# Kernel optimization log

Hardware: AMD Instinct MI355X
Metric: run time of the kernel (lower is better)

The kernel has to match this reference:

```python
import jax, jax.numpy as jnp
import numpy as np

EMBED_DIM = 768
NUM_HEADS = 12
HEAD_DIM = EMBED_DIM // NUM_HEADS
B, S = 2, 2048


def setup_inputs() -> dict:
    key = jax.random.key(0)
    k1, k2, k3, k4, k5 = jax.random.split(key, 5)
    scale = 1.0 / np.sqrt(EMBED_DIM)
    return {
        "x": jax.random.normal(k1, (B, S, EMBED_DIM), dtype=jnp.float32),
        "w_qkv": jax.random.normal(k2, (EMBED_DIM, 3 * EMBED_DIM), dtype=jnp.float32) * scale,
        "b_qkv": jax.random.normal(k3, (3 * EMBED_DIM,), dtype=jnp.float32) * 0.01,
        "w_proj": jax.random.normal(k4, (EMBED_DIM, EMBED_DIM), dtype=jnp.float32) * scale,
        "b_proj": jax.random.normal(k5, (EMBED_DIM,), dtype=jnp.float32) * 0.01,
    }


def reference(x, w_qkv, b_qkv, w_proj, b_proj):
    b, s, e = x.shape
    h, d = NUM_HEADS, HEAD_DIM
    # fused QKV projection: [b, s, 3, h, d]
    qkv = (x @ w_qkv + b_qkv).reshape(b, s, 3, h, d)
    q = qkv[:, :, 0].transpose(0, 2, 1, 3)  # [b, h, s, d]
    k = qkv[:, :, 1].transpose(0, 2, 1, 3)
    v = qkv[:, :, 2].transpose(0, 2, 1, 3)
    scores = jnp.einsum("bhqd,bhkd->bhqk", q, k) * (d ** -0.5)
    attn = jax.nn.softmax(scores, axis=-1)  # dropout is identity in eval mode
    out = jnp.einsum("bhqk,bhkd->bhqd", attn, v)
    out = out.transpose(0, 2, 1, 3).reshape(b, s, e)
    return out @ w_proj + b_proj
```

## Files before the change

### kernel.cpp

```cpp
#include <hip/hip_runtime.h>
#include <hip/hip_bf16.h>


typedef __bf16 bf16x8 __attribute__((ext_vector_type(8)));
typedef float f32x4 __attribute__((ext_vector_type(4)));
typedef unsigned short ushortx8 __attribute__((ext_vector_type(8)));
typedef unsigned short ushortx4 __attribute__((ext_vector_type(4)));

#define EMB 768
#define SEQ 2048
#define NHEAD 12
#define HDIM 64
#define MROWS 4096
#define NQKV 2304
#define QSCALE 0.18033688011112042f

static __device__ __forceinline__ unsigned short b16(float f) {
  __hip_bfloat16 h = __float2bfloat16(f);
  return __builtin_bit_cast(unsigned short, h);
}

static __device__ __forceinline__ void gld16(const void* g, void* l) {
  __builtin_amdgcn_global_load_lds((const __attribute__((address_space(1))) void*)g,
                                   (__attribute__((address_space(3))) void*)l, 16, 0, 0);
}

__global__ __launch_bounds__(256) void k_prep(
    const float* __restrict__ x, const float* __restrict__ wqkv, const float* __restrict__ wproj,
    unsigned short* __restrict__ xb, unsigned short* __restrict__ wqkvT,
    unsigned short* __restrict__ wprojT) {
  __shared__ float t[64][65];
  const int bid = blockIdx.x;
  const int tid = threadIdx.x;
  if (bid < 1536) {
    int i = (bid * 256 + tid) * 8;
    f32x4 v0 = *(const f32x4*)(x + i);
    f32x4 v1 = *(const f32x4*)(x + i + 4);
    ushortx8 o;
    o[0] = b16(v0[0]); o[1] = b16(v0[1]); o[2] = b16(v0[2]); o[3] = b16(v0[3]);
    o[4] = b16(v1[0]); o[5] = b16(v1[1]); o[6] = b16(v1[2]); o[7] = b16(v1[3]);
    *(ushortx8*)(xb + i) = o;
    return;
  }
  const float* in; unsigned short* out; int N, bx, by;
  if (bid < 1536 + 432) { in = wqkv;  out = wqkvT;  N = NQKV; int r = bid - 1536; bx = r % 36; by = r / 36; }
  else                  { in = wproj; out = wprojT; N = EMB;  int r = bid - 1968; bx = r % 12; by = r / 12; }
  const int n0 = bx * 64, k0 = by * 64;
  const int xx = tid & 63, y0 = tid >> 6;
  #pragma unroll
  for (int i = 0; i < 16; ++i) { int r = y0 * 16 + i; t[r][xx] = in[(size_t)(k0 + r) * N + n0 + xx]; }
  __syncthreads();
  const int ks = tid & 7;
  const int nr0 = tid >> 3;
  #pragma unroll
  for (int i = 0; i < 2; ++i) {
    int nr = nr0 + i * 32;
    ushortx8 o;
    #pragma unroll
    for (int j = 0; j < 8; ++j) o[j] = b16(t[ks * 8 + j][nr]);
    *(ushortx8*)(out + (size_t)(n0 + nr) * EMB + k0 + ks * 8) = o;
  }
}

static __device__ __forceinline__ void gemm_tile_128(
    const unsigned short* __restrict__ A, const unsigned short* __restrict__ B,
    int K, int bm, int bn, char* lA, char* lB, f32x4 acc[4][4]) {
  const int tid = threadIdx.x, lane = tid & 63, w = tid >> 6;
  const int l15 = lane & 15, lg = lane >> 4;
  const int wm = w >> 1, wn = w & 1;
  #pragma unroll
  for (int m = 0; m < 4; ++m)
    #pragma unroll
    for (int n = 0; n < 4; ++n)
      acc[m][n] = (f32x4){0.f, 0.f, 0.f, 0.f};

  const int srow = w * 32 + (lane >> 3);
  const int glog = (lane & 7) ^ (lane >> 3);
  const size_t abase = (size_t)(bm * 128 + srow) * K + glog * 8;
  const size_t bbase = (size_t)(bn * 128 + srow) * K + glog * 8;
  const char* aB = lA + (wm * 64 + l15) * 128;
  const char* bB = lB + (wn * 64 + l15) * 128;
  const int rsw = (l15 & 7) << 4;

  const int T = K >> 6;
  {
    char* ad = lA + w * 4096; char* bd = lB + w * 4096;
    #pragma unroll
    for (int j = 0; j < 4; ++j) {
      gld16(A + abase + (size_t)j * 8 * K, ad + j * 1024);
      gld16(B + bbase + (size_t)j * 8 * K, bd + j * 1024);
    }
  }
  for (int t = 0; t < T; ++t) {
    const int cur = t & 1;
    if (t + 1 < T) {
      const int k1 = (t + 1) << 6;
      char* ad = lA + (cur ^ 1) * 16384 + w * 4096;
      char* bd = lB + (cur ^ 1) * 16384 + w * 4096;
      #pragma unroll
      for (int j = 0; j < 4; ++j) {
        gld16(A + abase + (size_t)j * 8 * K + k1, ad + j * 1024);
        gld16(B + bbase + (size_t)j * 8 * K + k1, bd + j * 1024);
      }
      asm volatile("s_waitcnt vmcnt(8)" ::: "memory");
    } else {
      asm volatile("s_waitcnt vmcnt(0)" ::: "memory");
    }
    __builtin_amdgcn_s_barrier();
    const char* ab = aB + cur * 16384;
    const char* bb = bB + cur * 16384;
    bf16x8 af[2][4], bfr[2][4];
    #pragma unroll
    for (int kk = 0; kk < 2; ++kk) {
      #pragma unroll
      for (int m = 0; m < 4; ++m)
        af[kk][m] = *(const bf16x8*)(ab + m * 2048 + (((kk * 4 + lg) * 16) ^ rsw));
      #pragma unroll
      for (int n = 0; n < 4; ++n)
        bfr[kk][n] = *(const bf16x8*)(bb + n * 2048 + (((kk * 4 + lg) * 16) ^ rsw));
    }
    #pragma unroll
    for (int kk = 0; kk < 2; ++kk)
      #pragma unroll
      for (int m = 0; m < 4; ++m)
        #pragma unroll
        for (int n = 0; n < 4; ++n)
          acc[m][n] = __builtin_amdgcn_mfma_f32_16x16x32_bf16(af[kk][m], bfr[kk][n], acc[m][n], 0, 0, 0);
    if (t + 1 < T) __builtin_amdgcn_s_barrier();
  }
}

static __device__ __forceinline__ int kvperm(int s) {
  return (s & ~0x1C) | ((s & 0x0C) << 1) | ((s & 0x10) >> 2);
}

__global__ __launch_bounds__(256) void k_gemm_qkv(
    const unsigned short* __restrict__ Xb, const unsigned short* __restrict__ Wt,
    const float* __restrict__ bias,
    unsigned short* __restrict__ Qb, unsigned short* __restrict__ Kb,
    unsigned short* __restrict__ VTb) {
  __shared__ __align__(16) char Alds[2 * 16384];
  __shared__ __align__(16) char Blds[2 * 16384];
  f32x4 acc[4][4];
  const int bm = blockIdx.x, bn = blockIdx.y;
  gemm_tile_128(Xb, Wt, EMB, bm, bn, Alds, Blds, acc);
  const int tid = threadIdx.x, lane = tid & 63, w = tid >> 6;
  const int l15 = lane & 15, lg = lane >> 4, wm = w >> 1, wn = w & 1;
  const int treg = bn / 6;
  if (treg < 2) {
    #pragma unroll
    for (int m = 0; m < 4; ++m)
      #pragma unroll
      for (int n = 0; n < 4; ++n)
        #pragma unroll
        for (int r = 0; r < 4; ++r) {
          int gr = bm * 128 + wm * 64 + m * 16 + lg * 4 + r;
          int gc = bn * 128 + wn * 64 + n * 16 + l15;
          float v = acc[m][n][r] + bias[gc];
          int rem = gc - treg * 768;
          int h = rem >> 6, d = rem & 63;
          int b = gr >> 11, s = gr & 2047;
          size_t off = ((size_t)(b * 12 + h) * 2048 + s) * 64 + d;
          if (treg == 0) Qb[off] = b16(v * QSCALE);
          else           Kb[off] = b16(v);
        }
  } else {
    #pragma unroll
    for (int m = 0; m < 4; ++m)
      #pragma unroll
      for (int n = 0; n < 4; ++n) {
        int gr0 = bm * 128 + wm * 64 + m * 16 + lg * 4;
        int gc = bn * 128 + wn * 64 + n * 16 + l15;
        int rem = gc - 1536;
        int h = rem >> 6, d = rem & 63;
        int b = gr0 >> 11, s0 = gr0 & 2047;
        int sp0 = kvperm(s0);
        ushortx4 o;
        #pragma unroll
        for (int r = 0; r < 4; ++r) o[r] = b16(acc[m][n][r] + bias[gc]);
        *(ushortx4*)(VTb + ((size_t)(b * 12 + h) * 64 + d) * 2048 + sp0) = o;
      }
  }
}

__global__ __launch_bounds__(256) void k_gemm_proj(
    const unsigned short* __restrict__ Ab, const unsigned short* __restrict__ Wt,
    const float* __restrict__ bias, float* __restrict__ out) {
  __shared__ __align__(16) char Alds[2 * 16384];
  __shared__ __align__(16) char Blds[2 * 16384];
  f32x4 acc[4][4];
  const int bm = blockIdx.x, bn = blockIdx.y;
  gemm_tile_128(Ab, Wt, EMB, bm, bn, Alds, Blds, acc);
  const int tid = threadIdx.x, lane = tid & 63, w = tid >> 6;
  const int l15 = lane & 15, lg = lane >> 4, wm = w >> 1, wn = w & 1;
  #pragma unroll
  for (int m = 0; m < 4; ++m)
    #pragma unroll
    for (int n = 0; n < 4; ++n)
      #pragma unroll
      for (int r = 0; r < 4; ++r) {
        int gr = bm * 128 + wm * 64 + m * 16 + lg * 4 + r;
        int gc = bn * 128 + wn * 64 + n * 16 + l15;
        out[(size_t)gr * EMB + gc] = acc[m][n][r] + bias[gc];
      }
}

__global__ __launch_bounds__(256) void k_attn(
    const unsigned short* __restrict__ Qg, const unsigned short* __restrict__ Kg,
    const unsigned short* __restrict__ VTg, unsigned short* __restrict__ AO) {
  __shared__ __align__(16) char KL[3 * 8192];
  __shared__ __align__(16) char VTL[3 * 8192];
  const int bid = blockIdx.x;
  const int slot = bid >> 3;
  const int bh = (bid & 7) * 3 + slot / 32;
  const int qt = slot & 31;
  const int b = bh / 12, h = bh % 12;
  const size_t base = (size_t)bh * (SEQ * HDIM);
  const int tid = threadIdx.x, lane = tid & 63, w = tid >> 6;
  const int l15 = lane & 15, lg = lane >> 4;
  const int swz = (l15 & 7) << 4;

  bf16x8 qf[2];
  {
    const size_t qoff = base + (size_t)(qt * 64 + w * 16 + l15) * 64 + lg * 8;
    qf[0] = *(const bf16x8*)(Qg + qoff);
    qf[1] = *(const bf16x8*)(Qg + qoff + 32);
  }

  const int srow0 = tid >> 3;
  const int scg0 = (tid & 7) ^ (srow0 & 7);
  const int scg1 = (tid & 7) ^ ((srow0 + 32) & 7);

  #define ASTAGE(tt, buf) do {                                                         \
    const int kv_ = (tt) * 64;                                                         \
    char* kd_ = KL + (buf) * 8192 + w * 1024;                                          \
    char* vd_ = VTL + (buf) * 8192 + w * 1024;                                         \
    gld16(Kg + base + (size_t)(kv_ + srow0) * 64 + scg0 * 8,           kd_);           \
    gld16(Kg + base + (size_t)(kv_ + srow0 + 32) * 64 + scg1 * 8,      kd_ + 4096);    \
    gld16(VTg + base + (size_t)srow0 * 2048 + kv_ + scg0 * 8,          vd_);           \
    gld16(VTg + base + (size_t)(srow0 + 32) * 2048 + kv_ + scg1 * 8,   vd_ + 4096);    \
  } while (0)

  f32x4 Oacc[4];
  #pragma unroll
  for (int nd = 0; nd < 4; ++nd) Oacc[nd] = (f32x4){0.f, 0.f, 0.f, 0.f};
  float l_ = 0.f;

  ASTAGE(0, 0);
  ASTAGE(1, 1);
  asm volatile("s_waitcnt vmcnt(4)" ::: "memory");
  __builtin_amdgcn_s_barrier();

  int cur = 0, pre = 2;
  for (int t = 0; t < 32; ++t) {
    if (t + 2 < 32) ASTAGE(t + 2, pre);
    const char* kb = KL + cur * 8192;
    const char* vb = VTL + cur * 8192;

    f32x4 sv[4];
    __builtin_amdgcn_s_setprio(1);
    #pragma unroll
    for (int n = 0; n < 4; ++n) {
      const char* rb = kb + (n * 16 + l15) * 128;
      bf16x8 kf0 = *(const bf16x8*)(rb + ((lg * 16) ^ swz));
      bf16x8 kf1 = *(const bf16x8*)(rb + ((64 + lg * 16) ^ swz));
      f32x4 z = (f32x4){0.f, 0.f, 0.f, 0.f};
      z = __builtin_amdgcn_mfma_f32_16x16x32_bf16(kf0, qf[0], z, 0, 0, 0);
      sv[n] = __builtin_amdgcn_mfma_f32_16x16x32_bf16(kf1, qf[1], z, 0, 0, 0);
    }

    #pragma unroll
    for (int c = 0; c < 2; ++c) {
      ushortx8 up;
      #pragma unroll
      for (int j = 0; j < 4; ++j) {
        float pa = __builtin_amdgcn_exp2f(sv[2 * c][j]);
        float pb = __builtin_amdgcn_exp2f(sv[2 * c + 1][j]);
        l_ += pa + pb;
        up[j] = b16(pa);
        up[4 + j] = b16(pb);
      }
      bf16x8 pfB = __builtin_bit_cast(bf16x8, up);
      #pragma unroll
      for (int nd = 0; nd < 4; ++nd) {
        const char* vr = vb + (nd * 16 + l15) * 128;
        bf16x8 vf = *(const bf16x8*)(vr + ((c * 64 + lg * 16) ^ swz));
        Oacc[nd] = __builtin_amdgcn_mfma_f32_16x16x32_bf16(vf, pfB, Oacc[nd], 0, 0, 0);
      }
    }
    __builtin_amdgcn_s_setprio(0);

    if (t < 31) {
      if (t < 30) asm volatile("s_waitcnt vmcnt(4)" ::: "memory");
      else        asm volatile("s_waitcnt vmcnt(0)" ::: "memory");
      __builtin_amdgcn_s_barrier();
    }
    cur = (cur == 2) ? 0 : cur + 1;
    pre = (pre == 2) ? 0 : pre + 1;
  }
  #undef ASTAGE

  l_ += __shfl_xor(l_, 16);
  l_ += __shfl_xor(l_, 32);
  const float rl = 1.0f / l_;
  const int q = qt * 64 + w * 16 + l15;
  #pragma unroll
  for (int nd = 0; nd < 4; ++nd) {
    ushortx4 o;
    #pragma unroll
    for (int r = 0; r < 4; ++r) o[r] = b16(Oacc[nd][r] * rl);
    *(ushortx4*)(AO + ((size_t)(b * 2048 + q)) * EMB + h * 64 + nd * 16 + lg * 4) = o;
  }
}

extern "C" void kernel_launch(void* const* d_in, const int* in_sizes, int n_in,
                              void* d_out, int out_size, void* d_ws, size_t ws_size,
                              hipStream_t stream) {
  const float* x     = (const float*)d_in[0];
  const float* wqkv  = (const float*)d_in[1];
  const float* bqkv  = (const float*)d_in[2];
  const float* wproj = (const float*)d_in[3];
  const float* bproj = (const float*)d_in[4];
  float* out = (float*)d_out;
  char* ws = (char*)d_ws;

  unsigned short* xb     = (unsigned short*)(ws + 0);
  unsigned short* wqkvT  = (unsigned short*)(ws + 6291456);
  unsigned short* wprojT = (unsigned short*)(ws + 9830400);
  unsigned short* Qb     = (unsigned short*)(ws + 11010048);
  unsigned short* Kb     = (unsigned short*)(ws + 17301504);
  unsigned short* VTb    = (unsigned short*)(ws + 23592960);
  unsigned short* AOb    = (unsigned short*)(ws + 29884416);

  k_prep<<<2112, 256, 0, stream>>>(x, wqkv, wproj, xb, wqkvT, wprojT);
  k_gemm_qkv<<<dim3(MROWS / 128, NQKV / 128), 256, 0, stream>>>(xb, wqkvT, bqkv, Qb, Kb, VTb);
  k_attn<<<24 * (SEQ / 64), 256, 0, stream>>>(Qb, Kb, VTb, AOb);
  k_gemm_proj<<<dim3(MROWS / 128, EMB / 128), 256, 0, stream>>>(AOb, wprojT, bproj, out);
}
```

Before: 89.21 us.

## Compute softmax row sums via MFMA with ones and remap GEMM block order per XCD

The attention kernel no longer sums the exponentiated scores with scalar adds and cross-lane shuffles. Instead it issues one extra MFMA per chunk that multiplies a bf16 ones vector by the P fragment, so the row sums land in an accumulator. This moves VALU adds off the exp path at the cost of MFMA work and summing bf16-rounded probabilities. Both GEMM kernels also switch to a 1D grid with a swizzled block-to-tile mapping, so that blocks placed on the same XCD share row tiles and reuse L2.

```diff
diff --git a/kernel.cpp b/kernel.cpp
--- a/kernel.cpp
+++ b/kernel.cpp
@@ -142,7 +142,10 @@
   __shared__ __align__(16) char Alds[2 * 16384];
   __shared__ __align__(16) char Blds[2 * 16384];
   f32x4 acc[4][4];
-  const int bm = blockIdx.x, bn = blockIdx.y;
+  const int id = blockIdx.x;
+  const int kq = id >> 3;
+  const int bn = kq % 18;
+  const int bm = (id & 7) * 4 + kq / 18;
   gemm_tile_128(Xb, Wt, EMB, bm, bn, Alds, Blds, acc);
   const int tid = threadIdx.x, lane = tid & 63, w = tid >> 6;
   const int l15 = lane & 15, lg = lane >> 4, wm = w >> 1, wn = w & 1;
@@ -189,7 +192,10 @@
   __shared__ __align__(16) char Alds[2 * 16384];
   __shared__ __align__(16) char Blds[2 * 16384];
   f32x4 acc[4][4];
-  const int bm = blockIdx.x, bn = blockIdx.y;
+  const int id = blockIdx.x;
+  const int kq = id >> 3;
+  const int bn = kq % 6;
+  const int bm = (id & 7) * 4 + kq / 6;
   gemm_tile_128(Ab, Wt, EMB, bm, bn, Alds, Blds, acc);
   const int tid = threadIdx.x, lane = tid & 63, w = tid >> 6;
   const int l15 = lane & 15, lg = lane >> 4, wm = w >> 1, wn = w & 1;
@@ -241,10 +247,15 @@
     gld16(VTg + base + (size_t)(srow0 + 32) * 2048 + kv_ + scg1 * 8,   vd_ + 4096);    \
   } while (0)
 
+  ushortx8 os;
+  #pragma unroll
+  for (int j = 0; j < 8; ++j) os[j] = 0x3F80;
+  const bf16x8 onesf = __builtin_bit_cast(bf16x8, os);
+
   f32x4 Oacc[4];
   #pragma unroll
   for (int nd = 0; nd < 4; ++nd) Oacc[nd] = (f32x4){0.f, 0.f, 0.f, 0.f};
-  float l_ = 0.f;
+  f32x4 Lacc = (f32x4){0.f, 0.f, 0.f, 0.f};
 
   ASTAGE(0, 0);
   ASTAGE(1, 1);
@@ -274,13 +285,11 @@
       ushortx8 up;
       #pragma unroll
       for (int j = 0; j < 4; ++j) {
-        float pa = __builtin_amdgcn_exp2f(sv[2 * c][j]);
-        float pb = __builtin_amdgcn_exp2f(sv[2 * c + 1][j]);
-        l_ += pa + pb;
-        up[j] = b16(pa);
-        up[4 + j] = b16(pb);
+        up[j]     = b16(__builtin_amdgcn_exp2f(sv[2 * c][j]));
+        up[4 + j] = b16(__builtin_amdgcn_exp2f(sv[2 * c + 1][j]));
       }
       bf16x8 pfB = __builtin_bit_cast(bf16x8, up);
+      Lacc = __builtin_amdgcn_mfma_f32_16x16x32_bf16(onesf, pfB, Lacc, 0, 0, 0);
       #pragma unroll
       for (int nd = 0; nd < 4; ++nd) {
         const char* vr = vb + (nd * 16 + l15) * 128;
@@ -300,9 +309,7 @@
   }
   #undef ASTAGE
 
-  l_ += __shfl_xor(l_, 16);
-  l_ += __shfl_xor(l_, 32);
-  const float rl = 1.0f / l_;
+  const float rl = 1.0f / Lacc[0];
   const int q = qt * 64 + w * 16 + l15;
   #pragma unroll
   for (int nd = 0; nd < 4; ++nd) {
@@ -333,7 +340,7 @@
   unsigned short* AOb    = (unsigned short*)(ws + 29884416);
 
   k_prep<<<2112, 256, 0, stream>>>(x, wqkv, wproj, xb, wqkvT, wprojT);
-  k_gemm_qkv<<<dim3(MROWS / 128, NQKV / 128), 256, 0, stream>>>(xb, wqkvT, bqkv, Qb, Kb, VTb);
+  k_gemm_qkv<<<576, 256, 0, stream>>>(xb, wqkvT, bqkv, Qb, Kb, VTb);
   k_attn<<<24 * (SEQ / 64), 256, 0, stream>>>(Qb, Kb, VTb, AOb);
-  k_gemm_proj<<<dim3(MROWS / 128, EMB / 128), 256, 0, stream>>>(AOb, wprojT, bproj, out);
-}
+  k_gemm_proj<<<192, 256, 0, stream>>>(AOb, wprojT, bproj, out);
+}
```

Result: no change. 90.98 us (+2.0%).

## Split attention waves over query and key halves to reuse K/V fragments

Applied to the files above, without the earlier changes.

Each wave of the attention kernel now covers 32 query rows and half of each 64-key tile instead of 16 query rows and the full tile. Every K and V fragment read from LDS therefore feeds two query blocks, which halves the LDS read traffic per MFMA. The partial outputs and row sums from the two key halves are combined through LDS in an epilogue, which adds a reduction step and extra accumulator registers. The probabilities are also packed to bf16 with a v_cvt_pk_bf16_f32 instruction that converts two floats at once, in place of separate per-element conversions.

```diff
diff --git a/kernel.cpp b/kernel.cpp
--- a/kernel.cpp
+++ b/kernel.cpp
@@ -6,6 +6,7 @@
 typedef float f32x4 __attribute__((ext_vector_type(4)));
 typedef unsigned short ushortx8 __attribute__((ext_vector_type(8)));
 typedef unsigned short ushortx4 __attribute__((ext_vector_type(4)));
+typedef unsigned int uintx4 __attribute__((ext_vector_type(4)));
 
 #define EMB 768
 #define SEQ 2048
@@ -18,6 +19,12 @@
 static __device__ __forceinline__ unsigned short b16(float f) {
   __hip_bfloat16 h = __float2bfloat16(f);
   return __builtin_bit_cast(unsigned short, h);
+}
+
+static __device__ __forceinline__ unsigned int cvtpk(float lo, float hi) {
+  unsigned int r;
+  asm("v_cvt_pk_bf16_f32 %0, %1, %2" : "=v"(r) : "v"(lo), "v"(hi));
+  return r;
 }
 
 static __device__ __forceinline__ void gld16(const void* g, void* l) {
@@ -208,8 +215,9 @@
 __global__ __launch_bounds__(256) void k_attn(
     const unsigned short* __restrict__ Qg, const unsigned short* __restrict__ Kg,
     const unsigned short* __restrict__ VTg, unsigned short* __restrict__ AO) {
-  __shared__ __align__(16) char KL[3 * 8192];
-  __shared__ __align__(16) char VTL[3 * 8192];
+  __shared__ __align__(16) char LDSbuf[49152];
+  char* KL  = LDSbuf;
+  char* VTL = LDSbuf + 24576;
   const int bid = blockIdx.x;
   const int slot = bid >> 3;
   const int bh = (bid & 7) * 3 + slot / 32;
@@ -218,13 +226,16 @@
   const size_t base = (size_t)bh * (SEQ * HDIM);
   const int tid = threadIdx.x, lane = tid & 63, w = tid >> 6;
   const int l15 = lane & 15, lg = lane >> 4;
+  const int qh = w >> 1, kh = w & 1;
   const int swz = (l15 & 7) << 4;
 
-  bf16x8 qf[2];
+  bf16x8 qf[2][2];
   {
-    const size_t qoff = base + (size_t)(qt * 64 + w * 16 + l15) * 64 + lg * 8;
-    qf[0] = *(const bf16x8*)(Qg + qoff);
-    qf[1] = *(const bf16x8*)(Qg + qoff + 32);
+    const size_t qoff = base + (size_t)(qt * 64 + qh * 32 + l15) * 64 + lg * 8;
+    qf[0][0] = *(const bf16x8*)(Qg + qoff);
+    qf[0][1] = *(const bf16x8*)(Qg + qoff + 32);
+    qf[1][0] = *(const bf16x8*)(Qg + qoff + 1024);
+    qf[1][1] = *(const bf16x8*)(Qg + qoff + 1024 + 32);
   }
 
   const int srow0 = tid >> 3;
@@ -241,10 +252,12 @@
     gld16(VTg + base + (size_t)(srow0 + 32) * 2048 + kv_ + scg1 * 8,   vd_ + 4096);    \
   } while (0)
 
-  f32x4 Oacc[4];
-  #pragma unroll
-  for (int nd = 0; nd < 4; ++nd) Oacc[nd] = (f32x4){0.f, 0.f, 0.f, 0.f};
-  float l_ = 0.f;
+  f32x4 acc[2][4];
+  #pragma unroll
+  for (int n = 0; n < 2; ++n)
+    #pragma unroll
+    for (int nd = 0; nd < 4; ++nd) acc[n][nd] = (f32x4){0.f, 0.f, 0.f, 0.f};
+  float lsum[2] = {0.f, 0.f};
 
   ASTAGE(0, 0);
   ASTAGE(1, 1);
@@ -257,36 +270,48 @@
     const char* kb = KL + cur * 8192;
     const char* vb = VTL + cur * 8192;
 
-    f32x4 sv[4];
     __builtin_amdgcn_s_setprio(1);
-    #pragma unroll
-    for (int n = 0; n < 4; ++n) {
-      const char* rb = kb + (n * 16 + l15) * 128;
-      bf16x8 kf0 = *(const bf16x8*)(rb + ((lg * 16) ^ swz));
-      bf16x8 kf1 = *(const bf16x8*)(rb + ((64 + lg * 16) ^ swz));
-      f32x4 z = (f32x4){0.f, 0.f, 0.f, 0.f};
-      z = __builtin_amdgcn_mfma_f32_16x16x32_bf16(kf0, qf[0], z, 0, 0, 0);
-      sv[n] = __builtin_amdgcn_mfma_f32_16x16x32_bf16(kf1, qf[1], z, 0, 0, 0);
-    }
-
-    #pragma unroll
-    for (int c = 0; c < 2; ++c) {
-      ushortx8 up;
-      #pragma unroll
-      for (int j = 0; j < 4; ++j) {
-        float pa = __builtin_amdgcn_exp2f(sv[2 * c][j]);
-        float pb = __builtin_amdgcn_exp2f(sv[2 * c + 1][j]);
-        l_ += pa + pb;
-        up[j] = b16(pa);
-        up[4 + j] = b16(pb);
+    bf16x8 kf[2][2], vf[4];
+    #pragma unroll
+    for (int n2 = 0; n2 < 2; ++n2) {
+      const char* rb = kb + (kh * 32 + n2 * 16 + l15) * 128;
+      kf[n2][0] = *(const bf16x8*)(rb + ((lg * 16) ^ swz));
+      kf[n2][1] = *(const bf16x8*)(rb + ((64 + lg * 16) ^ swz));
+    }
+    #pragma unroll
+    for (int nd = 0; nd < 4; ++nd)
+      vf[nd] = *(const bf16x8*)(vb + (nd * 16 + l15) * 128 + ((kh * 64 + lg * 16) ^ swz));
+
+    f32x4 sv[2][2];
+    #pragma unroll
+    for (int n = 0; n < 2; ++n)
+      #pragma unroll
+      for (int n2 = 0; n2 < 2; ++n2) {
+        f32x4 z = (f32x4){0.f, 0.f, 0.f, 0.f};
+        z = __builtin_amdgcn_mfma_f32_16x16x32_bf16(kf[n2][0], qf[n][0], z, 0, 0, 0);
+        sv[n][n2] = __builtin_amdgcn_mfma_f32_16x16x32_bf16(kf[n2][1], qf[n][1], z, 0, 0, 0);
       }
-      bf16x8 pfB = __builtin_bit_cast(bf16x8, up);
-      #pragma unroll
-      for (int nd = 0; nd < 4; ++nd) {
-        const char* vr = vb + (nd * 16 + l15) * 128;
-        bf16x8 vf = *(const bf16x8*)(vr + ((c * 64 + lg * 16) ^ swz));
-        Oacc[nd] = __builtin_amdgcn_mfma_f32_16x16x32_bf16(vf, pfB, Oacc[nd], 0, 0, 0);
-      }
+
+    #pragma unroll
+    for (int n = 0; n < 2; ++n) {
+      float p0 = __builtin_amdgcn_exp2f(sv[n][0][0]);
+      float p1 = __builtin_amdgcn_exp2f(sv[n][0][1]);
+      float p2 = __builtin_amdgcn_exp2f(sv[n][0][2]);
+      float p3 = __builtin_amdgcn_exp2f(sv[n][0][3]);
+      float p4 = __builtin_amdgcn_exp2f(sv[n][1][0]);
+      float p5 = __builtin_amdgcn_exp2f(sv[n][1][1]);
+      float p6 = __builtin_amdgcn_exp2f(sv[n][1][2]);
+      float p7 = __builtin_amdgcn_exp2f(sv[n][1][3]);
+      lsum[n] += ((p0 + p1) + (p2 + p3)) + ((p4 + p5) + (p6 + p7));
+      uintx4 uw;
+      uw[0] = cvtpk(p0, p1);
+      uw[1] = cvtpk(p2, p3);
+      uw[2] = cvtpk(p4, p5);
+      uw[3] = cvtpk(p6, p7);
+      bf16x8 pf = __builtin_bit_cast(bf16x8, uw);
+      #pragma unroll
+      for (int nd = 0; nd < 4; ++nd)
+        acc[n][nd] = __builtin_amdgcn_mfma_f32_16x16x32_bf16(vf[nd], pf, acc[n][nd], 0, 0, 0);
     }
     __builtin_amdgcn_s_setprio(0);
 
@@ -300,16 +325,39 @@
   }
   #undef ASTAGE
 
-  l_ += __shfl_xor(l_, 16);
-  l_ += __shfl_xor(l_, 32);
-  const float rl = 1.0f / l_;
-  const int q = qt * 64 + w * 16 + l15;
-  #pragma unroll
-  for (int nd = 0; nd < 4; ++nd) {
-    ushortx4 o;
-    #pragma unroll
-    for (int r = 0; r < 4; ++r) o[r] = b16(Oacc[nd][r] * rl);
-    *(ushortx4*)(AO + ((size_t)(b * 2048 + q)) * EMB + h * 64 + nd * 16 + lg * 4) = o;
+  #pragma unroll
+  for (int n = 0; n < 2; ++n) {
+    lsum[n] += __shfl_xor(lsum[n], 16);
+    lsum[n] += __shfl_xor(lsum[n], 32);
+  }
+  __syncthreads();
+  float* scr = (float*)LDSbuf;
+  float* lscr = scr + 8192;
+  #pragma unroll
+  for (int n = 0; n < 2; ++n)
+    #pragma unroll
+    for (int nd = 0; nd < 4; ++nd)
+      *(f32x4*)(scr + ((w * 2 + n) * 4 + nd) * 256 + lane * 4) = acc[n][nd];
+  if (lane < 16) {
+    lscr[w * 32 + l15] = lsum[0];
+    lscr[w * 32 + 16 + l15] = lsum[1];
+  }
+  __syncthreads();
+  {
+    const int pw = w ^ 1;
+    const int n = kh;
+    const float lp = lscr[pw * 32 + n * 16 + l15];
+    const float rl = 1.0f / (lsum[n] + lp);
+    const int q = qt * 64 + qh * 32 + n * 16 + l15;
+    unsigned short* aor = AO + ((size_t)(b * 2048 + q)) * EMB + h * 64;
+    #pragma unroll
+    for (int nd = 0; nd < 4; ++nd) {
+      f32x4 part = *(const f32x4*)(scr + ((pw * 2 + n) * 4 + nd) * 256 + lane * 4);
+      ushortx4 o;
+      #pragma unroll
+      for (int r = 0; r < 4; ++r) o[r] = b16((acc[n][nd][r] + part[r]) * rl);
+      *(ushortx4*)(aor + nd * 16 + lg * 4) = o;
+    }
   }
 }
 
```

After: 92.30 us. 3.5% more time.

## Use 64x64 tiles with XCD-aware block mapping in output projection GEMM

Applied to the files above, without the earlier changes.

Replaces the 128x128-tile projection GEMM (192 blocks) with a dedicated 64x64-tile kernel launched as 768 blocks, so more of the GPU's compute units get work. Block ids are remapped so that consecutive ids spread across the 8 XCDs while each XCD handles a contiguous range of rows, which should improve L2 reuse. The kernel keeps double-buffered direct-to-LDS loads with a swizzle. The cost is more redundant A/B loads per output element and a smaller MFMA count per barrier.

```diff
diff --git a/kernel.cpp b/kernel.cpp
--- a/kernel.cpp
+++ b/kernel.cpp
@@ -186,21 +186,83 @@
 __global__ __launch_bounds__(256) void k_gemm_proj(
     const unsigned short* __restrict__ Ab, const unsigned short* __restrict__ Wt,
     const float* __restrict__ bias, float* __restrict__ out) {
-  __shared__ __align__(16) char Alds[2 * 16384];
-  __shared__ __align__(16) char Blds[2 * 16384];
-  f32x4 acc[4][4];
-  const int bm = blockIdx.x, bn = blockIdx.y;
-  gemm_tile_128(Ab, Wt, EMB, bm, bn, Alds, Blds, acc);
+  __shared__ __align__(16) char Alds[2 * 8192];
+  __shared__ __align__(16) char Blds[2 * 8192];
+  const int id = blockIdx.x;
+  const int k = id >> 3;
+  const int bn = k % 12;
+  const int bm = (id & 7) * 8 + k / 12;
   const int tid = threadIdx.x, lane = tid & 63, w = tid >> 6;
-  const int l15 = lane & 15, lg = lane >> 4, wm = w >> 1, wn = w & 1;
-  #pragma unroll
-  for (int m = 0; m < 4; ++m)
-    #pragma unroll
-    for (int n = 0; n < 4; ++n)
+  const int l15 = lane & 15, lg = lane >> 4;
+  const int wm = w >> 1, wn = w & 1;
+  f32x4 acc[2][2];
+  #pragma unroll
+  for (int m = 0; m < 2; ++m)
+    #pragma unroll
+    for (int n = 0; n < 2; ++n)
+      acc[m][n] = (f32x4){0.f, 0.f, 0.f, 0.f};
+
+  const int srow = w * 8 + (lane >> 3);
+  const int glog = (lane & 7) ^ (lane >> 3);
+  const size_t abase  = (size_t)(bm * 64 + srow) * EMB + glog * 8;
+  const size_t abase2 = abase + (size_t)32 * EMB;
+  const size_t bbase  = (size_t)(bn * 64 + srow) * EMB + glog * 8;
+  const size_t bbase2 = bbase + (size_t)32 * EMB;
+  const char* aB = (char*)Alds + (wm * 32 + l15) * 128;
+  const char* bB = (char*)Blds + (wn * 32 + l15) * 128;
+  const int rsw = (l15 & 7) << 4;
+
+  #define G2STAGE(k1, buf) do {                                          \
+    char* ad_ = (char*)Alds + (buf) * 8192 + w * 1024;                   \
+    char* bd_ = (char*)Blds + (buf) * 8192 + w * 1024;                   \
+    gld16(Ab + abase + (k1), ad_);                                       \
+    gld16(Ab + abase2 + (k1), ad_ + 4096);                               \
+    gld16(Wt + bbase + (k1), bd_);                                       \
+    gld16(Wt + bbase2 + (k1), bd_ + 4096);                               \
+  } while (0)
+
+  G2STAGE(0, 0);
+  const int T = EMB >> 6;
+  for (int t = 0; t < T; ++t) {
+    const int cur = t & 1;
+    if (t + 1 < T) {
+      G2STAGE((t + 1) << 6, cur ^ 1);
+      asm volatile("s_waitcnt vmcnt(4)" ::: "memory");
+    } else {
+      asm volatile("s_waitcnt vmcnt(0)" ::: "memory");
+    }
+    __builtin_amdgcn_s_barrier();
+    const char* ab = aB + cur * 8192;
+    const char* bb = bB + cur * 8192;
+    bf16x8 af[2][2], bfr[2][2];
+    #pragma unroll
+    for (int kk = 0; kk < 2; ++kk) {
+      #pragma unroll
+      for (int m = 0; m < 2; ++m)
+        af[kk][m] = *(const bf16x8*)(ab + m * 2048 + (((kk * 4 + lg) * 16) ^ rsw));
+      #pragma unroll
+      for (int n = 0; n < 2; ++n)
+        bfr[kk][n] = *(const bf16x8*)(bb + n * 2048 + (((kk * 4 + lg) * 16) ^ rsw));
+    }
+    #pragma unroll
+    for (int kk = 0; kk < 2; ++kk)
+      #pragma unroll
+      for (int m = 0; m < 2; ++m)
+        #pragma unroll
+        for (int n = 0; n < 2; ++n)
+          acc[m][n] = __builtin_amdgcn_mfma_f32_16x16x32_bf16(af[kk][m], bfr[kk][n], acc[m][n], 0, 0, 0);
+    if (t + 1 < T) __builtin_amdgcn_s_barrier();
+  }
+  #undef G2STAGE
+
+  #pragma unroll
+  for (int m = 0; m < 2; ++m)
+    #pragma unroll
+    for (int n = 0; n < 2; ++n)
       #pragma unroll
       for (int r = 0; r < 4; ++r) {
-        int gr = bm * 128 + wm * 64 + m * 16 + lg * 4 + r;
-        int gc = bn * 128 + wn * 64 + n * 16 + l15;
+        int gr = bm * 64 + wm * 32 + m * 16 + lg * 4 + r;
+        int gc = bn * 64 + wn * 32 + n * 16 + l15;
         out[(size_t)gr * EMB + gc] = acc[m][n][r] + bias[gc];
       }
 }
@@ -335,5 +397,5 @@
   k_prep<<<2112, 256, 0, stream>>>(x, wqkv, wproj, xb, wqkvT, wprojT);
   k_gemm_qkv<<<dim3(MROWS / 128, NQKV / 128), 256, 0, stream>>>(xb, wqkvT, bqkv, Qb, Kb, VTb);
   k_attn<<<24 * (SEQ / 64), 256, 0, stream>>>(Qb, Kb, VTb, AOb);
-  k_gemm_proj<<<dim3(MROWS / 128, EMB / 128), 256, 0, stream>>>(AOb, wprojT, bproj, out);
-}
+  k_gemm_proj<<<768, 256, 0, stream>>>(AOb, wprojT, bproj, out);
+}
```

After: 86.85 us (median of 2 runs). -2.7%, faster.
